# Kernel tuning notes

Hardware: AMD Instinct MI355X
Metric: run time of the kernel (lower is better)

The kernel has to match this reference:

```python
import jax, jax.numpy as jnp
import numpy as np
import math

B, N, D = 2, 4096, 1024
NUM_LAYERS = 12
INIT_RANGE = 0.02


def setup_inputs() -> dict:
    key = jax.random.key(0)
    k1, k2 = jax.random.split(key)
    hidden_states = jax.random.normal(k1, (B, N, D), dtype=jnp.float32)
    std = INIT_RANGE / math.sqrt(2.0 * NUM_LAYERS * D)
    queries = jax.random.normal(k2, (D, D), dtype=jnp.float32) * std
    return {"hidden_states": hidden_states, "queries": queries}


def reference(hidden_states, queries):
    # Q = F.linear(X, W) = X @ W^T  -> [B, N, D]
    q = jnp.einsum('bnd,ed->bne', hidden_states, queries)
    # pre_attn = Q @ X^T  -> [B, N, N]
    pre_attn = jnp.einsum('bne,bme->bnm', q, hidden_states)
    # attention = pre_attn @ X  -> [B, N, D]
    attention = jnp.einsum('bnm,bmd->bnd', pre_attn, hidden_states)
    return attention
```

## Files before the change

kernel.cpp:

```cpp
#include <hip/hip_runtime.h>
#include <hip/hip_bf16.h>
#include <stdint.h>

using bf16 = __hip_bfloat16;
typedef __attribute__((ext_vector_type(8))) short short8;
typedef __attribute__((ext_vector_type(4))) float f32x4;

#define BM 128
#define BK 32

__device__ __forceinline__ void g2lds16(const void* g, void* l) {
    __builtin_amdgcn_global_load_lds(
        (const __attribute__((address_space(1))) void*)g,
        (__attribute__((address_space(3))) void*)l,
        16, 0, 0);
}

__device__ __forceinline__ short f2bs(float x) {
    union { bf16 h; short s; } u;
    u.h = __float2bfloat16(x);
    return u.s;
}

__device__ __forceinline__ int bswz(int row, int cg) { return cg ^ ((row >> 1) & 3); }
__device__ __forceinline__ int fswz(int row, int cg) { return cg ^ (row & 7); }

__global__ __launch_bounds__(256)
void transpose_cvt(const float* __restrict__ src, ushort* __restrict__ dstT,
                   ushort* __restrict__ dstN,
                   int R, int C, long sstride, long dstrideT, long dstrideN)
{
    __shared__ __align__(16) ushort t[64][72];
    const float* s = src + (size_t)blockIdx.z * sstride;
    ushort*      dT = dstT + (size_t)blockIdx.z * dstrideT;
    const int r0 = blockIdx.y * 64, c0 = blockIdx.x * 64;
    const int tid = threadIdx.x;
#pragma unroll
    for (int ii = 0; ii < 4; ++ii) {
        int idx = ii * 256 + tid;
        int r = idx >> 4, c4 = (idx & 15) * 4;
        float4 v = *(const float4*)&s[(size_t)(r0 + r) * C + c0 + c4];
        union { ushort u[4]; uint2 q; } o;
        o.u[0] = (ushort)f2bs(v.x); o.u[1] = (ushort)f2bs(v.y);
        o.u[2] = (ushort)f2bs(v.z); o.u[3] = (ushort)f2bs(v.w);
        *(uint2*)&t[r][c4] = o.q;
        if (dstN) {
            ushort* dN = dstN + (size_t)blockIdx.z * dstrideN;
            *(uint2*)&dN[(size_t)(r0 + r) * C + c0 + c4] = o.q;
        }
    }
    __syncthreads();
#pragma unroll
    for (int ii = 0; ii < 2; ++ii) {
        int idx = ii * 256 + tid;
        int c = idx >> 3, r8 = (idx & 7) * 8;
        union { ushort u[8]; uint4 v; } tmp;
#pragma unroll
        for (int j = 0; j < 8; ++j) tmp.u[j] = t[r8 + j][c];
        *(uint4*)&dT[(size_t)(c0 + c) * R + r0 + r8] = tmp.v;
    }
}

template <int MODE, int A_F32, int NFRAG>
__global__ __launch_bounds__(256)
void gemm_bt(const void* __restrict__ Av, const bf16* __restrict__ B,
             void* __restrict__ Cv, int M, int N, int K, int kChunks,
             long sA, long sB, long sC)
{
    constexpr int BN  = 32 * NFRAG;
    constexpr int BSH = BN / 64;
    __shared__ __align__(16) bf16 lA[BM * BK * (A_F32 ? 2 : 1)];
    __shared__ __align__(16) bf16 lB[BN * BK];

    const int z     = blockIdx.z;
    const int batch = z / kChunks;
    const int chunk = z - batch * kChunks;
    const int kLen  = K / kChunks;
    const int k0    = chunk * kLen;

    const int m0 = blockIdx.y * BM;
    const int n0 = blockIdx.x * BN;

    const int tid  = threadIdx.x;
    const int lane = tid & 63;
    const int wave = tid >> 6;
    const int wr   = wave >> 1, wc = wave & 1;
    const int ml   = lane & 15;
    const int q    = lane >> 4;

    const bf16* Bb = B + (size_t)batch * sB;
    const bf16* bp[BSH];
#pragma unroll
    for (int s = 0; s < BSH; ++s) {
        int idx = s * 256 + tid;
        int row = idx >> 2, cg = idx & 3;
        bp[s] = Bb + (size_t)(n0 + row) * K + k0 + 8 * bswz(row, cg);
    }

    const float* a32[4];
    const bf16*  a16[2];
    if constexpr (A_F32) {
        const float* Ab = (const float*)Av + (size_t)batch * sA;
#pragma unroll
        for (int s = 0; s < 4; ++s) {
            int idx = s * 256 + tid;
            int row = idx >> 3, cg = idx & 7;
            a32[s] = Ab + (size_t)(m0 + row) * K + k0 + 4 * fswz(row, cg);
        }
    } else {
        const bf16* Ab = (const bf16*)Av + (size_t)batch * sA;
#pragma unroll
        for (int s = 0; s < 2; ++s) {
            int idx = s * 256 + tid;
            int row = idx >> 2, cg = idx & 3;
            a16[s] = Ab + (size_t)(m0 + row) * K + k0 + 8 * bswz(row, cg);
        }
    }

    f32x4 acc[4][NFRAG] = {};

    const int nk = kLen / BK;
    for (int kt = 0; kt < nk; ++kt) {
        if constexpr (A_F32) {
            float* lAf = (float*)lA;
#pragma unroll
            for (int s = 0; s < 4; ++s) {
                g2lds16(a32[s], &lAf[(s * 256 + tid) * 4]);
                a32[s] += BK;
            }
        } else {
#pragma unroll
            for (int s = 0; s < 2; ++s) {
                g2lds16(a16[s], &lA[(s * 256 + tid) * 8]);
                a16[s] += BK;
            }
        }
#pragma unroll
        for (int s = 0; s < BSH; ++s) {
            g2lds16(bp[s], &lB[(s * 256 + tid) * 8]);
            bp[s] += BK;
        }
        __syncthreads();

        short8 af[4], bfr[NFRAG];
#pragma unroll
        for (int i = 0; i < 4; ++i) {
            const int rA = wr * 64 + i * 16 + ml;
            if constexpr (A_F32) {
                const float* lAf = (const float*)lA;
                float4 x0 = *(const float4*)&lAf[rA * 32 + 4 * fswz(rA, 2 * q)];
                float4 x1 = *(const float4*)&lAf[rA * 32 + 4 * fswz(rA, 2 * q + 1)];
                af[i][0] = f2bs(x0.x); af[i][1] = f2bs(x0.y);
                af[i][2] = f2bs(x0.z); af[i][3] = f2bs(x0.w);
                af[i][4] = f2bs(x1.x); af[i][5] = f2bs(x1.y);
                af[i][6] = f2bs(x1.z); af[i][7] = f2bs(x1.w);
            } else {
                af[i] = *(const short8*)&lA[rA * 32 + 8 * bswz(rA, q)];
            }
        }
#pragma unroll
        for (int j = 0; j < NFRAG; ++j) {
            const int rB = wc * (16 * NFRAG) + j * 16 + ml;
            bfr[j] = *(const short8*)&lB[rB * 32 + 8 * bswz(rB, q)];
        }
#pragma unroll
        for (int mi = 0; mi < 4; ++mi)
#pragma unroll
            for (int nj = 0; nj < NFRAG; ++nj)
                acc[mi][nj] = __builtin_amdgcn_mfma_f32_16x16x32_bf16(
                    af[mi], bfr[nj], acc[mi][nj], 0, 0, 0);
        __syncthreads();
    }

#pragma unroll
    for (int mi = 0; mi < 4; ++mi)
#pragma unroll
        for (int nj = 0; nj < NFRAG; ++nj)
#pragma unroll
            for (int r = 0; r < 4; ++r) {
                int row = m0 + wr * 64 + mi * 16 + q * 4 + r;
                int col = n0 + wc * (16 * NFRAG) + nj * 16 + ml;
                if constexpr (MODE == 1) {
                    float* Cf = (float*)Cv + (size_t)batch * sC;
                    atomicAdd(&Cf[(size_t)row * N + col], acc[mi][nj][r]);
                } else if constexpr (MODE == 0) {
                    ushort* Cb = (ushort*)Cv + (size_t)batch * sC;
                    Cb[(size_t)row * N + col] = (ushort)f2bs(acc[mi][nj][r]);
                } else {
                    float* Cf = (float*)Cv + (size_t)batch * sC;
                    Cf[(size_t)row * N + col] = acc[mi][nj][r];
                }
            }
}

extern "C" void kernel_launch(void* const* d_in, const int* in_sizes, int n_in,
                              void* d_out, int out_size, void* d_ws, size_t ws_size,
                              hipStream_t stream)
{
    const int B = 2, N = 4096, D = 1024;
    const float* X = (const float*)d_in[0];
    const float* W = (const float*)d_in[1];
    float* out = (float*)d_out;

    char* ob = (char*)d_out;
    char* ws = (char*)d_ws;
    ushort* Xt = (ushort*)ob;
    float*  Gf = (float*)(ob + (16ll << 20));
    ushort* Wt = (ushort*)(ob + (28ll << 20));

    const bool bigws = ws_size >= (20ull << 20);
    ushort* Xb = bigws ? (ushort*)ws : nullptr;
    ushort* Mt = (ushort*)(ws + (bigws ? (16ll << 20) : 0));

    transpose_cvt<<<dim3(D / 64, N / 64, B), 256, 0, stream>>>(
        X, Xt, Xb, N, D, (long)N * D, (long)D * N, (long)N * D);
    transpose_cvt<<<dim3(D / 64, D / 64, 1), 256, 0, stream>>>(
        W, Wt, nullptr, D, D, 0, 0, 0);
    (void)hipMemsetAsync(Gf, 0, (size_t)B * D * D * sizeof(float), stream);
    gemm_bt<1, 0, 4><<<dim3(D / 128, D / BM, B * 4), 256, 0, stream>>>(
        (const void*)Xt, (const bf16*)Xt, Gf, D, D, N, 4,
        (long)D * N, (long)D * N, (long)D * D);
    gemm_bt<0, 1, 2><<<dim3(D / 64, D / BM, B), 256, 0, stream>>>(
        (const void*)Gf, (const bf16*)Wt, Mt, D, D, D, 1,
        (long)D * D, 0, (long)D * D);
    if (bigws) {
        gemm_bt<2, 0, 4><<<dim3(D / 128, N / BM, B), 256, 0, stream>>>(
            (const void*)Xb, (const bf16*)Mt, out, N, D, D, 1,
            (long)N * D, (long)D * D, (long)N * D);
    } else {
        gemm_bt<2, 1, 4><<<dim3(D / 128, N / BM, B), 256, 0, stream>>>(
            (const void*)X, (const bf16*)Mt, out, N, D, D, 1,
            (long)N * D, (long)D * D, (long)N * D);
    }
}
```

Baseline: 206.3 us.

## Double-buffer LDS tiles and swizzle block order in GEMM kernel

Adds two LDS buffers so the global-to-LDS loads for the next K tile are issued before the MFMA work on the current tile, with one barrier per iteration instead of two. It also remaps the flat block index so consecutive blocks are spread in strides of eight, which is meant to improve L2 locality across tiles. The cost is double the shared memory per block, which may reduce occupancy, and the remap assumes the grid size is divisible by eight. A single barrier after compute relies on the async loads being complete by the time of the next read, and the global_load_lds vmcnt wait that the barrier provides is the only guard.

```diff
diff --git a/kernel.cpp b/kernel.cpp
--- a/kernel.cpp
+++ b/kernel.cpp
@@ -69,8 +69,9 @@
 {
     constexpr int BN  = 32 * NFRAG;
     constexpr int BSH = BN / 64;
-    __shared__ __align__(16) bf16 lA[BM * BK * (A_F32 ? 2 : 1)];
-    __shared__ __align__(16) bf16 lB[BN * BK];
+    constexpr int ANE = BM * BK * (A_F32 ? 2 : 1);
+    __shared__ __align__(16) bf16 lA[2][ANE];
+    __shared__ __align__(16) bf16 lB[2][BN * BK];
 
     const int z     = blockIdx.z;
     const int batch = z / kChunks;
@@ -78,8 +79,12 @@
     const int kLen  = K / kChunks;
     const int k0    = chunk * kLen;
 
-    const int m0 = blockIdx.y * BM;
-    const int n0 = blockIdx.x * BN;
+    const int gx  = gridDim.x;
+    int flat = blockIdx.y * gx + blockIdx.x;
+    const int cpx = (gx * gridDim.y) >> 3;
+    flat = (flat & 7) * cpx + (flat >> 3);
+    const int m0 = (flat / gx) * BM;
+    const int n0 = (flat - (flat / gx) * gx) * BN;
 
     const int tid  = threadIdx.x;
     const int lane = tid & 63;
@@ -119,10 +124,9 @@
 
     f32x4 acc[4][NFRAG] = {};
 
-    const int nk = kLen / BK;
-    for (int kt = 0; kt < nk; ++kt) {
+    auto stage = [&](int buf) {
         if constexpr (A_F32) {
-            float* lAf = (float*)lA;
+            float* lAf = (float*)lA[buf];
 #pragma unroll
             for (int s = 0; s < 4; ++s) {
                 g2lds16(a32[s], &lAf[(s * 256 + tid) * 4]);
@@ -131,23 +135,26 @@
         } else {
 #pragma unroll
             for (int s = 0; s < 2; ++s) {
-                g2lds16(a16[s], &lA[(s * 256 + tid) * 8]);
+                g2lds16(a16[s], &lA[buf][(s * 256 + tid) * 8]);
                 a16[s] += BK;
             }
         }
 #pragma unroll
         for (int s = 0; s < BSH; ++s) {
-            g2lds16(bp[s], &lB[(s * 256 + tid) * 8]);
+            g2lds16(bp[s], &lB[buf][(s * 256 + tid) * 8]);
             bp[s] += BK;
         }
-        __syncthreads();
-
+    };
+
+    auto compute = [&](int buf) {
+        const bf16* cA = lA[buf];
+        const bf16* cB = lB[buf];
         short8 af[4], bfr[NFRAG];
 #pragma unroll
         for (int i = 0; i < 4; ++i) {
             const int rA = wr * 64 + i * 16 + ml;
             if constexpr (A_F32) {
-                const float* lAf = (const float*)lA;
+                const float* lAf = (const float*)cA;
                 float4 x0 = *(const float4*)&lAf[rA * 32 + 4 * fswz(rA, 2 * q)];
                 float4 x1 = *(const float4*)&lAf[rA * 32 + 4 * fswz(rA, 2 * q + 1)];
                 af[i][0] = f2bs(x0.x); af[i][1] = f2bs(x0.y);
@@ -155,13 +162,13 @@
                 af[i][4] = f2bs(x1.x); af[i][5] = f2bs(x1.y);
                 af[i][6] = f2bs(x1.z); af[i][7] = f2bs(x1.w);
             } else {
-                af[i] = *(const short8*)&lA[rA * 32 + 8 * bswz(rA, q)];
+                af[i] = *(const short8*)&cA[rA * 32 + 8 * bswz(rA, q)];
             }
         }
 #pragma unroll
         for (int j = 0; j < NFRAG; ++j) {
             const int rB = wc * (16 * NFRAG) + j * 16 + ml;
-            bfr[j] = *(const short8*)&lB[rB * 32 + 8 * bswz(rB, q)];
+            bfr[j] = *(const short8*)&cB[rB * 32 + 8 * bswz(rB, q)];
         }
 #pragma unroll
         for (int mi = 0; mi < 4; ++mi)
@@ -169,8 +176,19 @@
             for (int nj = 0; nj < NFRAG; ++nj)
                 acc[mi][nj] = __builtin_amdgcn_mfma_f32_16x16x32_bf16(
                     af[mi], bfr[nj], acc[mi][nj], 0, 0, 0);
+    };
+
+    const int nk = kLen / BK;
+    stage(0);
+    __syncthreads();
+    int cur = 0;
+    for (int kt = 0; kt < nk - 1; ++kt) {
+        stage(cur ^ 1);
+        compute(cur);
         __syncthreads();
-    }
+        cur ^= 1;
+    }
+    compute(cur);
 
 #pragma unroll
     for (int mi = 0; mi < 4; ++mi)
```

After: 203.1 us. About the same (-1.5%).
